# Kernel tuning notes

Hardware: AMD Instinct MI355X
Metric: run time of the kernel (lower is better)

The kernel has to match this reference:

```python
import jax, jax.numpy as jnp
import numpy as np

N_DRUG = 846
D = 256          # embedding_num
K = 128          # neighbor_sample_size
N_REL = 200
N_ENT = 100000
BN_EPS = 1e-5


def setup_inputs() -> dict:
    key = jax.random.key(0)
    ks = jax.random.split(key, 12)
    drug_name = jnp.arange(N_DRUG, dtype=jnp.int64) if jax.config.jax_enable_x64 else jnp.arange(N_DRUG, dtype=jnp.int32)
    adj_tail = jax.random.randint(ks[0], (N_DRUG, K), 0, N_ENT)
    adj_relation = jax.random.randint(ks[1], (N_DRUG, K), 0, N_REL)
    drug_table = jax.random.normal(ks[2], (N_DRUG, D), dtype=jnp.float32)
    rela_table = jax.random.normal(ks[3], (N_REL, D), dtype=jnp.float32)
    ent_table = jax.random.normal(ks[4], (N_ENT, D), dtype=jnp.float32)
    W1 = jax.random.normal(ks[5], (N_DRUG, D, D), dtype=jnp.float32) * 0.05
    b1 = jax.random.normal(ks[6], (K, D), dtype=jnp.float32) * 0.05
    W2 = jax.random.normal(ks[7], (N_DRUG, D, D), dtype=jnp.float32) * 0.05
    b2 = jax.random.normal(ks[8], (K, D), dtype=jnp.float32) * 0.05
    # Linear(2D -> D), xavier-uniform weight, zero bias
    lim = np.sqrt(6.0 / (2 * D + D)).astype(np.float32)
    lin_w = jax.random.uniform(ks[9], (D, 2 * D), minval=-lim, maxval=lim, dtype=jnp.float32)
    lin_b = jnp.zeros((D,), dtype=jnp.float32)
    bn_gamma = jnp.ones((D,), dtype=jnp.float32)
    bn_beta = jnp.zeros((D,), dtype=jnp.float32)
    return {
        "drug_name": drug_name, "adj_tail": adj_tail, "adj_relation": adj_relation,
        "drug_table": drug_table, "rela_table": rela_table, "ent_table": ent_table,
        "W1": W1, "b1": b1, "W2": W2, "b2": b2,
        "lin_w": lin_w, "lin_b": lin_b, "bn_gamma": bn_gamma, "bn_beta": bn_beta,
    }


def reference(drug_name, adj_tail, adj_relation, drug_table, rela_table, ent_table,
              W1, b1, W2, b2, lin_w, lin_b, bn_gamma, bn_beta):
    drug_emb = drug_table[drug_name]                  # [N, D]
    rela_emb = rela_table[adj_relation]               # [N, K, D]
    ent_emb = ent_table[adj_tail]                     # [N, K, D]

    drug_rel = drug_emb[:, None, :] * rela_emb        # [N, K, D]
    h = jnp.einsum('nkd,nde->nke', drug_rel, W1) + b1 # per-drug bmm + bias
    h = jax.nn.relu(h)
    h = jnp.einsum('nkd,nde->nke', h, W2) + b2        # [N, K, D]

    score = jnp.sum(h, axis=-1, keepdims=True)        # [N, K, 1]
    score = jax.nn.softmax(score, axis=1)             # softmax over neighbors

    weighted_ent = jnp.einsum('nk,nkd->nd', score[..., 0], ent_emb)  # [N, D]
    drug_e = jnp.concatenate([weighted_ent, drug_emb], axis=1)       # [N, 2D]

    x = drug_e @ lin_w.T + lin_b                      # Linear(2D -> D)
    x = jax.nn.relu(x)
    # BatchNorm1d in training mode: biased batch statistics
    mean = jnp.mean(x, axis=0)
    var = jnp.var(x, axis=0)
    drug_f = bn_gamma * (x - mean) * jax.lax.rsqrt(var + BN_EPS) + bn_beta
    return drug_f
```

## Files before the change

### kernel.cpp

```cpp
#include <hip/hip_runtime.h>
#include <math.h>

#define NDRUG 846
#define DIM   256
#define KN    128

typedef _Float16 half8 __attribute__((ext_vector_type(8)));
typedef float f32x4 __attribute__((ext_vector_type(4)));

__global__ __launch_bounds__(256) void b2sum_kernel(const float* __restrict__ b2,
                                                    float* __restrict__ b2sum) {
    int row  = blockIdx.x * 4 + (threadIdx.x >> 6);
    int lane = threadIdx.x & 63;
    if (row >= KN) return;
    float4 v = *((const float4*)(b2 + (size_t)row * DIM) + lane);
    float s = v.x + v.y + v.z + v.w;
    #pragma unroll
    for (int off = 32; off >= 1; off >>= 1) s += __shfl_xor(s, off);
    if (lane == 0) b2sum[row] = s;
}

__global__ __launch_bounds__(256, 2) void gnn_main(
    const int* __restrict__ adj_rel,
    const float* __restrict__ drug_table, const float* __restrict__ rela_table,
    const float* __restrict__ W1, const float* __restrict__ b1,
    const float* __restrict__ W2, const float* __restrict__ b2sum,
    float* __restrict__ score_out)
{
    __shared__ __align__(16) half8 sB[8][8][64];
    __shared__ __align__(16) _Float16 sA[2][4][520];
    __shared__ float s_w2[DIM];
    __shared__ float s_scoreP[4][KN];
    __shared__ float s_red[8];

    const int n    = blockIdx.x;
    const int t    = threadIdx.x;
    const int wv   = t >> 6;
    const int lane = t & 63;

    const float* W1n   = W1 + (size_t)n * DIM * DIM;
    const float* W2n   = W2 + (size_t)n * DIM * DIM;
    const float* wbase = W1n + (size_t)(wv << 3) * DIM + lane;
    const int w2row0 = (wv << 1) + (lane >> 5);
    const int w2c    = lane & 31;

    const int kk = t >> 1, o0 = (t & 1) << 1;
    const int   rid     = adj_rel[(size_t)n * KN + kk];
    const float sc_init = b2sum[t & (KN - 1)];

    float P[4][8]; float4 Qa[4], Qb[4];
    #pragma unroll
    for (int s = 0; s < 4; ++s) {
        const float* p = wbase + (size_t)((s & 7) << 5) * DIM + ((s >> 3) << 6);
        #pragma unroll
        for (int j = 0; j < 8; ++j) P[s][j] = p[(size_t)j * DIM];
        const float4* wr = (const float4*)(W2n + (size_t)((s << 3) + w2row0) * DIM);
        Qa[s] = wr[w2c]; Qb[s] = wr[32 + w2c];
    }

    {
        const float* rrow = rela_table + (size_t)rid * DIM;
        const float* drow = drug_table + (size_t)n * DIM;
        #pragma unroll 2
        for (int s8 = 0; s8 < 8; ++s8) {
            #pragma unroll
            for (int i = 0; i < 2; ++i) {
                const int o  = o0 | i;
                const int db = (s8 << 5) + (o << 3);
                float4 p0 = *(const float4*)(rrow + db);
                float4 p1 = *(const float4*)(rrow + db + 4);
                float4 q0 = *(const float4*)(drow + db);
                float4 q1 = *(const float4*)(drow + db + 4);
                half8 h;
                h[0] = (_Float16)(p0.x * q0.x);
                h[1] = (_Float16)(p0.y * q0.y);
                h[2] = (_Float16)(p0.z * q0.z);
                h[3] = (_Float16)(p0.w * q0.w);
                h[4] = (_Float16)(p1.x * q1.x);
                h[5] = (_Float16)(p1.y * q1.y);
                h[6] = (_Float16)(p1.z * q1.z);
                h[7] = (_Float16)(p1.w * q1.w);
                sB[s8][kk >> 4][(kk & 15) | (o << 4)] = h;
            }
        }
    }

    const int kcol = lane & 15, quad = lane >> 4;
    f32x4 acc[8] = {};
    float sacc[8] = {0.f,0.f,0.f,0.f,0.f,0.f,0.f,0.f};
    const f32x4 fzero = {};

    #pragma unroll
    for (int ss = 0; ss < 32; ++ss) {
        const int rb = ss & 3;
        half8 hw;
        #pragma unroll
        for (int j = 0; j < 8; ++j) hw[j] = (_Float16)P[rb][j];
        *(half8*)&sA[ss & 1][lane >> 4][((lane & 15) | (wv << 4)) << 3] = hw;
        {
            float4 qa = Qa[rb], qb = Qb[rb];
            float wsum = (qa.x + qa.y + qa.z + qa.w) + (qb.x + qb.y + qb.z + qb.w);
            wsum += __shfl_xor(wsum, 1);
            wsum += __shfl_xor(wsum, 2);
            wsum += __shfl_xor(wsum, 4);
            wsum += __shfl_xor(wsum, 8);
            wsum += __shfl_xor(wsum, 16);
            if ((lane & 31) == 0) s_w2[(ss << 3) + w2row0] = wsum;
        }
        if (ss + 4 < 32) {
            const int sn = ss + 4;
            const float* p = wbase + (size_t)((sn & 7) << 5) * DIM + ((sn >> 3) << 6);
            #pragma unroll
            for (int j = 0; j < 8; ++j) P[rb][j] = p[(size_t)j * DIM];
            const float4* wr = (const float4*)(W2n + (size_t)((sn << 3) + w2row0) * DIM);
            Qa[rb] = wr[w2c]; Qb[rb] = wr[32 + w2c];
        }
        asm volatile("s_waitcnt lgkmcnt(0)\n\ts_barrier" ::: "memory");
        half8 af = *(const half8*)&sA[ss & 1][wv][(size_t)lane << 3];
        const int ds = ss & 7;
        #pragma unroll
        for (int kt = 0; kt < 8; ++kt) {
            half8 bf = sB[ds][kt][lane];
            acc[kt] = __builtin_amdgcn_mfma_f32_16x16x32_f16(af, bf, acc[kt], 0, 0, 0);
        }
        if (ds == 7) {
            const int c = ss >> 3;
            const int ebase = (c << 6) + (wv << 4) + (quad << 2);
            float4 ww = *(const float4*)(s_w2 + ebase);
            #pragma unroll
            for (int kt = 0; kt < 8; ++kt) {
                const int k = (kt << 4) + kcol;
                float4 bb = *(const float4*)(b1 + (size_t)k * DIM + ebase);
                f32x4 a = acc[kt];
                sacc[kt] += fmaxf(a[0] + bb.x, 0.f) * ww.x
                          + fmaxf(a[1] + bb.y, 0.f) * ww.y
                          + fmaxf(a[2] + bb.z, 0.f) * ww.z
                          + fmaxf(a[3] + bb.w, 0.f) * ww.w;
                acc[kt] = fzero;
            }
        }
    }

    #pragma unroll
    for (int kt = 0; kt < 8; ++kt) {
        float v = sacc[kt];
        v += __shfl_xor(v, 16);
        v += __shfl_xor(v, 32);
        if (lane < 16) s_scoreP[wv][(kt << 4) + lane] = v;
    }
    __syncthreads();
    float sc = -3.0e38f;
    if (t < KN)
        sc = sc_init + (s_scoreP[0][t] + s_scoreP[1][t]) + (s_scoreP[2][t] + s_scoreP[3][t]);

    float mx = sc;
    #pragma unroll
    for (int off = 32; off >= 1; off >>= 1) mx = fmaxf(mx, __shfl_xor(mx, off));
    if (lane == 0) s_red[wv] = mx;
    __syncthreads();
    float M = fmaxf(fmaxf(s_red[0], s_red[1]), fmaxf(s_red[2], s_red[3]));
    float ex = (t < KN) ? expf(sc - M) : 0.f;
    float ssum = ex;
    #pragma unroll
    for (int off = 32; off >= 1; off >>= 1) ssum += __shfl_xor(ssum, off);
    if (lane == 0) s_red[4 + wv] = ssum;
    __syncthreads();
    float S = (s_red[4] + s_red[5]) + (s_red[6] + s_red[7]);
    if (t < KN) score_out[(size_t)n * KN + t] = ex / S;
}

__global__ __launch_bounds__(256) void gather_kernel(
    const float* __restrict__ score, const int* __restrict__ adj_tail,
    const float* __restrict__ ent_table, const float* __restrict__ drug_table,
    float* __restrict__ drug_e)
{
    __shared__ float s_p[KN];
    __shared__ int   s_ti[KN];
    const int n = blockIdx.x, t = threadIdx.x;
    if (t < KN) {
        s_p[t]  = score[(size_t)n * KN + t];
        s_ti[t] = adj_tail[(size_t)n * KN + t];
    }
    __syncthreads();
    float a0=0.f,a1=0.f,a2=0.f,a3=0.f,a4=0.f,a5=0.f,a6=0.f,a7=0.f;
    for (int k = 0; k < KN; k += 8) {
        float v0 = ent_table[(size_t)s_ti[k + 0] * DIM + t];
        float v1 = ent_table[(size_t)s_ti[k + 1] * DIM + t];
        float v2 = ent_table[(size_t)s_ti[k + 2] * DIM + t];
        float v3 = ent_table[(size_t)s_ti[k + 3] * DIM + t];
        float v4 = ent_table[(size_t)s_ti[k + 4] * DIM + t];
        float v5 = ent_table[(size_t)s_ti[k + 5] * DIM + t];
        float v6 = ent_table[(size_t)s_ti[k + 6] * DIM + t];
        float v7 = ent_table[(size_t)s_ti[k + 7] * DIM + t];
        a0 += s_p[k + 0] * v0;  a1 += s_p[k + 1] * v1;
        a2 += s_p[k + 2] * v2;  a3 += s_p[k + 3] * v3;
        a4 += s_p[k + 4] * v4;  a5 += s_p[k + 5] * v5;
        a6 += s_p[k + 6] * v6;  a7 += s_p[k + 7] * v7;
    }
    drug_e[(size_t)n * 512 + t]       = ((a0 + a1) + (a2 + a3)) + ((a4 + a5) + (a6 + a7));
    drug_e[(size_t)n * 512 + DIM + t] = drug_table[(size_t)n * DIM + t];
}

__global__ __launch_bounds__(256) void linear_kernel(
    const float* __restrict__ drug_e, const float* __restrict__ lin_w,
    const float* __restrict__ lin_b,
    float* __restrict__ x, float* __restrict__ g_sum, float* __restrict__ g_sumsq)
{
    __shared__ __align__(16) float s_de[4][512];
    const int b = blockIdx.x, t = threadIdx.x;
    const int n0 = b * 4;
    #pragma unroll
    for (int ss = 0; ss < 2; ++ss) {
        int idx = ss * 256 + t;
        int row = idx >> 7, col4 = idx & 127;
        float4 v = make_float4(0.f, 0.f, 0.f, 0.f);
        if (n0 + row < NDRUG) v = *((const float4*)(drug_e + (size_t)(n0 + row) * 512) + col4);
        *(float4*)&s_de[row][col4 * 4] = v;
    }
    __syncthreads();
    float acc[4] = {};
    const float4* wrow = (const float4*)(lin_w + (size_t)t * 512);
    #pragma unroll 4
    for (int d4 = 0; d4 < 128; ++d4) {
        float4 w = wrow[d4];
        #pragma unroll
        for (int i = 0; i < 4; ++i) {
            float4 de = *(const float4*)&s_de[i][d4 * 4];
            acc[i] += w.x * de.x + w.y * de.y + w.z * de.z + w.w * de.w;
        }
    }
    float bias = lin_b[t];
    float psum = 0.f, psq = 0.f;
    #pragma unroll
    for (int i = 0; i < 4; ++i) {
        if (n0 + i < NDRUG) {
            float v = fmaxf(acc[i] + bias, 0.f);
            x[(size_t)(n0 + i) * DIM + t] = v;
            psum += v; psq += v * v;
        }
    }
    atomicAdd(&g_sum[t], psum);
    atomicAdd(&g_sumsq[t], psq);
}

__global__ __launch_bounds__(256) void bn_kernel(
    const float* __restrict__ x, const float* __restrict__ g_sum,
    const float* __restrict__ g_sumsq,
    const float* __restrict__ gamma, const float* __restrict__ beta,
    float* __restrict__ out)
{
    const int n = blockIdx.x, e = threadIdx.x;
    const float inv = 1.0f / (float)NDRUG;
    float mean = g_sum[e] * inv;
    float var  = fmaxf(g_sumsq[e] * inv - mean * mean, 0.f);
    float rstd = rsqrtf(var + 1e-5f);
    float v = x[(size_t)n * DIM + e];
    out[(size_t)n * DIM + e] = gamma[e] * (v - mean) * rstd + beta[e];
}

extern "C" void kernel_launch(void* const* d_in, const int* in_sizes, int n_in,
                              void* d_out, int out_size, void* d_ws, size_t ws_size,
                              hipStream_t stream) {
    const int*   adj_tail   = (const int*)d_in[1];
    const int*   adj_rel    = (const int*)d_in[2];
    const float* drug_table = (const float*)d_in[3];
    const float* rela_table = (const float*)d_in[4];
    const float* ent_table  = (const float*)d_in[5];
    const float* W1         = (const float*)d_in[6];
    const float* b1         = (const float*)d_in[7];
    const float* W2         = (const float*)d_in[8];
    const float* b2         = (const float*)d_in[9];
    const float* lin_w      = (const float*)d_in[10];
    const float* lin_b      = (const float*)d_in[11];
    const float* gamma      = (const float*)d_in[12];
    const float* beta       = (const float*)d_in[13];
    float* out = (float*)d_out;

    float* ws      = (float*)d_ws;
    float* b2sum   = ws;
    float* drug_e  = ws + 128;
    float* xbuf    = drug_e + (size_t)NDRUG * 512;
    float* score_w = xbuf;
    float* g_sum   = xbuf + (size_t)NDRUG * DIM;
    float* g_sumsq = g_sum + DIM;

    hipMemsetAsync(g_sum, 0, 2 * DIM * sizeof(float), stream);
    b2sum_kernel<<<KN / 4, 256, 0, stream>>>(b2, b2sum);
    gnn_main<<<NDRUG, 256, 0, stream>>>(adj_rel, drug_table, rela_table,
                                        W1, b1, W2, b2sum, score_w);
    gather_kernel<<<NDRUG, 256, 0, stream>>>(score_w, adj_tail, ent_table,
                                             drug_table, drug_e);
    linear_kernel<<<(NDRUG + 3) / 4, 256, 0, stream>>>(drug_e, lin_w, lin_b,
                                                       xbuf, g_sum, g_sumsq);
    bn_kernel<<<NDRUG, 256, 0, stream>>>(xbuf, g_sum, g_sumsq, gamma, beta, out);
}
```

Before: 585.7 us.

## Restructure W1 GEMM loop over d-chunks with all output tiles accumulated in registers

```diff
diff --git a/kernel.cpp b/kernel.cpp
--- a/kernel.cpp
+++ b/kernel.cpp
@@ -6,6 +6,7 @@
 #define KN    128
 
 typedef _Float16 half8 __attribute__((ext_vector_type(8)));
+typedef _Float16 half4 __attribute__((ext_vector_type(4)));
 typedef float f32x4 __attribute__((ext_vector_type(4)));
 
 __global__ __launch_bounds__(256) void b2sum_kernel(const float* __restrict__ b2,
@@ -27,8 +28,8 @@
     const float* __restrict__ W2, const float* __restrict__ b2sum,
     float* __restrict__ score_out)
 {
-    __shared__ __align__(16) half8 sB[8][8][64];
-    __shared__ __align__(16) _Float16 sA[2][4][520];
+    __shared__ __align__(16) _Float16 sA[2][256 * 32];
+    __shared__ __align__(16) half8 sB[2][8][64];
     __shared__ float s_w2[DIM];
     __shared__ float s_scoreP[4][KN];
     __shared__ float s_red[8];
@@ -38,106 +39,117 @@
     const int wv   = t >> 6;
     const int lane = t & 63;
 
-    const float* W1n   = W1 + (size_t)n * DIM * DIM;
-    const float* W2n   = W2 + (size_t)n * DIM * DIM;
-    const float* wbase = W1n + (size_t)(wv << 3) * DIM + lane;
-    const int w2row0 = (wv << 1) + (lane >> 5);
-    const int w2c    = lane & 31;
+    const float* W1n = W1 + (size_t)n * DIM * DIM;
+    const float* W2n = W2 + (size_t)n * DIM * DIM;
+    const float4* w1base = (const float4*)W1n + (size_t)(wv << 3) * 64 + lane;
+    const float4* w2base = (const float4*)W2n + (size_t)((wv << 3) + (lane >> 5)) * 64 + (lane & 31);
 
     const int kk = t >> 1, o0 = (t & 1) << 1;
     const int   rid     = adj_rel[(size_t)n * KN + kk];
     const float sc_init = b2sum[t & (KN - 1)];
-
-    float P[4][8]; float4 Qa[4], Qb[4];
-    #pragma unroll
-    for (int s = 0; s < 4; ++s) {
-        const float* p = wbase + (size_t)((s & 7) << 5) * DIM + ((s >> 3) << 6);
-        #pragma unroll
-        for (int j = 0; j < 8; ++j) P[s][j] = p[(size_t)j * DIM];
-        const float4* wr = (const float4*)(W2n + (size_t)((s << 3) + w2row0) * DIM);
-        Qa[s] = wr[w2c]; Qb[s] = wr[32 + w2c];
-    }
-
-    {
-        const float* rrow = rela_table + (size_t)rid * DIM;
-        const float* drow = drug_table + (size_t)n * DIM;
-        #pragma unroll 2
-        for (int s8 = 0; s8 < 8; ++s8) {
+    const float4* rrow = (const float4*)(rela_table + (size_t)rid * DIM);
+    const float4* drow = (const float4*)(drug_table + (size_t)n * DIM);
+
+    float4 P[8]; float4 Qa[4], Qb[4];
+    #pragma unroll
+    for (int k = 0; k < 8; ++k) P[k] = w1base[k * 64];
+    #pragma unroll
+    for (int p = 0; p < 4; ++p) { Qa[p] = w2base[p * 128]; Qb[p] = w2base[p * 128 + 32]; }
+
+    const int kE   = lane & 7;
+    const int kcol = lane & 15, quad = lane >> 4;
+    f32x4 acc[4][8] = {};
+
+    #pragma unroll 2
+    for (int s = 0; s < 8; ++s) {
+        const int buf = s & 1;
+        #pragma unroll
+        for (int i = 0; i < 4; ++i) {
+            const int e = (lane << 2) + i;
             #pragma unroll
-            for (int i = 0; i < 2; ++i) {
-                const int o  = o0 | i;
-                const int db = (s8 << 5) + (o << 3);
-                float4 p0 = *(const float4*)(rrow + db);
-                float4 p1 = *(const float4*)(rrow + db + 4);
-                float4 q0 = *(const float4*)(drow + db);
-                float4 q1 = *(const float4*)(drow + db + 4);
-                half8 h;
-                h[0] = (_Float16)(p0.x * q0.x);
-                h[1] = (_Float16)(p0.y * q0.y);
-                h[2] = (_Float16)(p0.z * q0.z);
-                h[3] = (_Float16)(p0.w * q0.w);
-                h[4] = (_Float16)(p1.x * q1.x);
-                h[5] = (_Float16)(p1.y * q1.y);
-                h[6] = (_Float16)(p1.z * q1.z);
-                h[7] = (_Float16)(p1.w * q1.w);
-                sB[s8][kk >> 4][(kk & 15) | (o << 4)] = h;
+            for (int h = 0; h < 2; ++h) {
+                half4 v;
+                v[0] = (_Float16)((&P[4 * h + 0].x)[i]);
+                v[1] = (_Float16)((&P[4 * h + 1].x)[i]);
+                v[2] = (_Float16)((&P[4 * h + 2].x)[i]);
+                v[3] = (_Float16)((&P[4 * h + 3].x)[i]);
+                const int Q = (wv << 1) + h;
+                *(half4*)&sA[buf][e * 32 + ((Q ^ kE) << 2)] = v;
             }
         }
-    }
-
-    const int kcol = lane & 15, quad = lane >> 4;
-    f32x4 acc[8] = {};
-    float sacc[8] = {0.f,0.f,0.f,0.f,0.f,0.f,0.f,0.f};
-    const f32x4 fzero = {};
-
-    #pragma unroll
-    for (int ss = 0; ss < 32; ++ss) {
-        const int rb = ss & 3;
-        half8 hw;
-        #pragma unroll
-        for (int j = 0; j < 8; ++j) hw[j] = (_Float16)P[rb][j];
-        *(half8*)&sA[ss & 1][lane >> 4][((lane & 15) | (wv << 4)) << 3] = hw;
-        {
-            float4 qa = Qa[rb], qb = Qb[rb];
-            float wsum = (qa.x + qa.y + qa.z + qa.w) + (qb.x + qb.y + qb.z + qb.w);
-            wsum += __shfl_xor(wsum, 1);
-            wsum += __shfl_xor(wsum, 2);
-            wsum += __shfl_xor(wsum, 4);
-            wsum += __shfl_xor(wsum, 8);
-            wsum += __shfl_xor(wsum, 16);
-            if ((lane & 31) == 0) s_w2[(ss << 3) + w2row0] = wsum;
-        }
-        if (ss + 4 < 32) {
-            const int sn = ss + 4;
-            const float* p = wbase + (size_t)((sn & 7) << 5) * DIM + ((sn >> 3) << 6);
+        if (s < 7) {
             #pragma unroll
-            for (int j = 0; j < 8; ++j) P[rb][j] = p[(size_t)j * DIM];
-            const float4* wr = (const float4*)(W2n + (size_t)((sn << 3) + w2row0) * DIM);
-            Qa[rb] = wr[w2c]; Qb[rb] = wr[32 + w2c];
+            for (int k = 0; k < 8; ++k) P[k] = w1base[(s + 1) * 2048 + k * 64];
+        }
+        #pragma unroll
+        for (int i2 = 0; i2 < 2; ++i2) {
+            const int o  = o0 | i2;
+            const int f4 = (s << 3) + (o << 1);
+            float4 p0 = rrow[f4], p1 = rrow[f4 + 1];
+            float4 q0 = drow[f4], q1 = drow[f4 + 1];
+            half8 hh;
+            hh[0] = (_Float16)(p0.x * q0.x);
+            hh[1] = (_Float16)(p0.y * q0.y);
+            hh[2] = (_Float16)(p0.z * q0.z);
+            hh[3] = (_Float16)(p0.w * q0.w);
+            hh[4] = (_Float16)(p1.x * q1.x);
+            hh[5] = (_Float16)(p1.y * q1.y);
+            hh[6] = (_Float16)(p1.z * q1.z);
+            hh[7] = (_Float16)(p1.w * q1.w);
+            sB[buf][kk >> 4][(kk & 15) | (o << 4)] = hh;
+        }
+        #pragma unroll
+        for (int p = 0; p < 4; ++p) {
+            float4 qa = Qa[p], qb = Qb[p];
+            float w = (qa.x + qa.y + qa.z + qa.w) + (qb.x + qb.y + qb.z + qb.w);
+            w += __shfl_xor(w, 1);
+            w += __shfl_xor(w, 2);
+            w += __shfl_xor(w, 4);
+            w += __shfl_xor(w, 8);
+            w += __shfl_xor(w, 16);
+            if ((lane & 31) == 0)
+                s_w2[(s << 5) + (wv << 3) + (p << 1) + (lane >> 5)] = w;
+        }
+        if (s < 7) {
+            #pragma unroll
+            for (int p = 0; p < 4; ++p) {
+                Qa[p] = w2base[(s + 1) * 2048 + p * 128];
+                Qb[p] = w2base[(s + 1) * 2048 + p * 128 + 32];
+            }
         }
         asm volatile("s_waitcnt lgkmcnt(0)\n\ts_barrier" ::: "memory");
-        half8 af = *(const half8*)&sA[ss & 1][wv][(size_t)lane << 3];
-        const int ds = ss & 7;
-        #pragma unroll
-        for (int kt = 0; kt < 8; ++kt) {
-            half8 bf = sB[ds][kt][lane];
-            acc[kt] = __builtin_amdgcn_mfma_f32_16x16x32_f16(af, bf, acc[kt], 0, 0, 0);
-        }
-        if (ds == 7) {
-            const int c = ss >> 3;
-            const int ebase = (c << 6) + (wv << 4) + (quad << 2);
-            float4 ww = *(const float4*)(s_w2 + ebase);
+        #pragma unroll
+        for (int c = 0; c < 4; ++c) {
+            const int e_l = ((c << 2) + wv) * 16 + kcol;
+            const int kEl = (e_l >> 2) & 7;
+            const int Q0  = quad << 1;
+            half4 a0 = *(const half4*)&sA[buf][e_l * 32 + ((Q0 ^ kEl) << 2)];
+            half4 a1 = *(const half4*)&sA[buf][e_l * 32 + (((Q0 + 1) ^ kEl) << 2)];
+            half8 af;
+            af[0] = a0[0]; af[1] = a0[1]; af[2] = a0[2]; af[3] = a0[3];
+            af[4] = a1[0]; af[5] = a1[1]; af[6] = a1[2]; af[7] = a1[3];
             #pragma unroll
             for (int kt = 0; kt < 8; ++kt) {
-                const int k = (kt << 4) + kcol;
-                float4 bb = *(const float4*)(b1 + (size_t)k * DIM + ebase);
-                f32x4 a = acc[kt];
-                sacc[kt] += fmaxf(a[0] + bb.x, 0.f) * ww.x
-                          + fmaxf(a[1] + bb.y, 0.f) * ww.y
-                          + fmaxf(a[2] + bb.z, 0.f) * ww.z
-                          + fmaxf(a[3] + bb.w, 0.f) * ww.w;
-                acc[kt] = fzero;
+                half8 bf = sB[buf][kt][lane];
+                acc[c][kt] = __builtin_amdgcn_mfma_f32_16x16x32_f16(af, bf, acc[c][kt], 0, 0, 0);
             }
+        }
+    }
+
+    float sacc[8] = {0.f,0.f,0.f,0.f,0.f,0.f,0.f,0.f};
+    #pragma unroll
+    for (int c = 0; c < 4; ++c) {
+        const int ebase = (c << 6) + (wv << 4) + (quad << 2);
+        float4 ww = *(const float4*)(s_w2 + ebase);
+        #pragma unroll
+        for (int kt = 0; kt < 8; ++kt) {
+            const int k = (kt << 4) + kcol;
+            float4 bb = *(const float4*)(b1 + (size_t)k * DIM + ebase);
+            f32x4 a = acc[c][kt];
+            sacc[kt] += fmaxf(a[0] + bb.x, 0.f) * ww.x
+                      + fmaxf(a[1] + bb.y, 0.f) * ww.y
+                      + fmaxf(a[2] + bb.z, 0.f) * ww.z
+                      + fmaxf(a[3] + bb.w, 0.f) * ww.w;
         }
     }
 
```

New measurement: 577.6 us. About the same (-1.4%).
